# Kernel optimization log

Measured on AMD Instinct MI355X. Metric: run time of the kernel, lower is better.

## Reference

```python
import jax, jax.numpy as jnp
import numpy as np

N = 4096      # n_patches / nodes
IN_FEAT = 512
EMBED = 512
HEADS = 8
HEAD_DIM = EMBED // HEADS
SCALING = HEAD_DIM ** -0.5


def setup_inputs() -> dict:
    key = jax.random.key(0)
    ks = jax.random.split(key, 7)
    x = jax.random.normal(ks[0], (N, IN_FEAT), dtype=jnp.float32)
    adj = jax.random.randint(ks[1], (N, N), 0, 2, dtype=jnp.int32)
    s = 0.04  # ~xavier scale for 512x512
    WQ = jax.random.normal(ks[2], (EMBED, IN_FEAT), dtype=jnp.float32) * s
    WK = jax.random.normal(ks[3], (EMBED, IN_FEAT), dtype=jnp.float32) * s
    WV = jax.random.normal(ks[4], (EMBED, IN_FEAT), dtype=jnp.float32) * s
    we = jax.random.normal(ks[5], (1, HEAD_DIM), dtype=jnp.float32) * 0.1
    be = jnp.zeros((1,), dtype=jnp.float32)
    return {"x": x, "adj": adj, "WQ": WQ, "WK": WK, "WV": WV, "we": we, "be": be}


def reference(x, adj, WQ, WK, WV, we, be):
    n = x.shape[0]
    # projections: [N, E] -> [H, N, head_dim]
    Q = (x @ WQ.T).reshape(n, HEADS, HEAD_DIM).transpose(1, 0, 2)
    K = (x @ WK.T).reshape(n, HEADS, HEAD_DIM).transpose(1, 0, 2)
    V = (x @ WV.T).reshape(n, HEADS, HEAD_DIM).transpose(1, 0, 2)
    # scores + per-query energy term: [H, N, N]
    energy = Q @ we.T + be                      # [H, N, 1]
    attn = jnp.einsum('hqd,hkd->hqk', Q, K) * SCALING + energy
    # adjacency mask (broadcast over heads)
    attn = attn + jnp.where(adj > 0, 0.0, -jnp.inf)
    attn = jax.nn.softmax(attn, axis=-1)
    # winner-take-all: one-hot at row max, divided by num_heads
    hard = (attn == jnp.max(attn, axis=-1, keepdims=True)).astype(jnp.float32) / HEADS
    out = jnp.einsum('hqk,hkd->hqd', hard, V)   # [H, N, head_dim]
    return out.transpose(1, 0, 2).reshape(n, EMBED)
```

## Files before the change

### kernel.cpp

```cpp
#include <hip/hip_runtime.h>
#include <hip/hip_bf16.h>
#include <float.h>
#include <stdint.h>

#define NPT    4096
#define EMB    512
#define NH     8
#define HD     64
#define KSPLIT 32

typedef __attribute__((ext_vector_type(8))) short bf16x8;
typedef __attribute__((ext_vector_type(4))) float f32x4;
typedef uint32_t u32;

__device__ __forceinline__ void async_ld16(const void* gsrc, void* ldst) {
    __builtin_amdgcn_global_load_lds(
        (const __attribute__((address_space(1))) u32*)gsrc,
        (__attribute__((address_space(3))) u32*)ldst, 16, 0, 0);
}

__device__ __forceinline__ void split3(float a, unsigned short& h,
                                       unsigned short& m, unsigned short& l) {
    __hip_bfloat16 bh = __float2bfloat16(a);
    float fh = __bfloat162float(bh);
    float r1 = a - fh;
    __hip_bfloat16 bm = __float2bfloat16(r1);
    float fm = __bfloat162float(bm);
    float r2 = r1 - fm;
    __hip_bfloat16 bl = __float2bfloat16(r2);
    h = *reinterpret_cast<unsigned short*>(&bh);
    m = *reinterpret_cast<unsigned short*>(&bm);
    l = *reinterpret_cast<unsigned short*>(&bl);
}

__global__ __launch_bounds__(256) void prep_kernel(const float* __restrict__ x,
                                                   const float* __restrict__ wq,
                                                   const float* __restrict__ wk,
                                                   const float* __restrict__ wv,
                                                   const int* __restrict__ adj,
                                                   unsigned short* __restrict__ xs,
                                                   unsigned short* __restrict__ wqs,
                                                   unsigned short* __restrict__ wks,
                                                   unsigned short* __restrict__ wvs,
                                                   unsigned* __restrict__ bits_t) {
    int y = blockIdx.y;
    size_t i = (size_t)blockIdx.x * 256 + threadIdx.x;
    if (y == 4) {
        int q = (int)(i >> 7), w = (int)i & 127;
        const int4* p = (const int4*)(adj + (size_t)q * NPT + w * 32);
        unsigned m = 0;
#pragma unroll
        for (int j = 0; j < 8; ++j) {
            int4 v = p[j];
            m |= (v.x != 0 ? 1u : 0u) << (j * 4 + 0);
            m |= (v.y != 0 ? 1u : 0u) << (j * 4 + 1);
            m |= (v.z != 0 ? 1u : 0u) << (j * 4 + 2);
            m |= (v.w != 0 ? 1u : 0u) << (j * 4 + 3);
        }
        bits_t[(size_t)w * NPT + q] = m;
    } else if (y == 0) {
        const size_t PL = (size_t)NPT * EMB;
        float4 v = ((const float4*)x)[i];
        int n  = (int)(i >> 7);
        int k0 = ((int)i & 127) * 4;
        int kc = k0 >> 5, kg = (k0 >> 3) & 3, dd = k0 & 7;
        size_t off = ((((size_t)(n >> 4) * 16 + kc) * 4 + kg) * 16 + (n & 15)) * 8 + dd;
        ushort4 h, m, l;
        split3(v.x, h.x, m.x, l.x);
        split3(v.y, h.y, m.y, l.y);
        split3(v.z, h.z, m.z, l.z);
        split3(v.w, h.w, m.w, l.w);
        *(ushort4*)(xs + off)          = h;
        *(ushort4*)(xs + PL + off)     = m;
        *(ushort4*)(xs + 2 * PL + off) = l;
    } else {
        const size_t WPL = 262144;
        if (i >= WPL / 4) return;
        const float* src = (y == 1) ? wq : (y == 2) ? wk : wv;
        unsigned short* dst = (y == 1) ? wqs : (y == 2) ? wks : wvs;
        float4 v = ((const float4*)src)[i];
        int e  = (int)(i >> 7);
        int k0 = ((int)i & 127) * 4;
        int ebk = e >> 6, el = e & 63;
        int kc = k0 >> 5, g = (k0 >> 3) & 3, dd = k0 & 7;
        size_t off = ((((size_t)ebk * 16 + kc) * 4 + g) * 64 + el) * 8 + dd;
        ushort4 h, m, l;
        split3(v.x, h.x, m.x, l.x);
        split3(v.y, h.y, m.y, l.y);
        split3(v.z, h.z, m.z, l.z);
        split3(v.w, h.w, m.w, l.w);
        *(ushort4*)(dst + off)           = h;
        *(ushort4*)(dst + WPL + off)     = m;
        *(ushort4*)(dst + 2 * WPL + off) = l;
    }
}

__global__ __launch_bounds__(256) void gemm_mfma(const unsigned short* __restrict__ xs,
                                                 const unsigned short* __restrict__ wqs,
                                                 const unsigned short* __restrict__ wks,
                                                 const unsigned short* __restrict__ wvs,
                                                 unsigned short* __restrict__ Q3,
                                                 unsigned short* __restrict__ K3,
                                                 float* __restrict__ V) {
    const size_t XPL = (size_t)NPT * EMB;
    const size_t WPL = 262144;
    const size_t OPL = (size_t)NH * NPT * HD;

    const int tn  = blockIdx.x;
    const int ebk = blockIdx.y;
    const int tid = threadIdx.x;
    const int wv = tid >> 6, lane = tid & 63;
    const int wn = wv & 1, we = wv >> 1;
    const int m = lane & 15, quad = lane >> 4;
    const int n0 = tn * 128 + wn * 64;
    const int e0 = we * 32;

    __shared__ __align__(16) unsigned short Ws[3 * 3 * 4 * 64 * 8];

    const unsigned short* Wz[3] = {wqs, wks, wvs};

    f32x4 acc[3][2][4];
#pragma unroll
    for (int z = 0; z < 3; ++z)
#pragma unroll
        for (int mt = 0; mt < 2; ++mt)
#pragma unroll
            for (int nt = 0; nt < 4; ++nt) acc[z][mt][nt] = (f32x4){0.f, 0.f, 0.f, 0.f};

#pragma unroll 1
    for (int kc = 0; kc < 16; ++kc) {
        __syncthreads();
#pragma unroll
        for (int i2 = 0; i2 < 9; ++i2) {
            int c = wv + 4 * i2;
            int z = c / 12, p = (c / 4) % 3, kg = c & 3;
            const unsigned short* src = Wz[z] + (size_t)p * WPL
                + (((size_t)ebk * 16 + kc) * 4 + kg) * 512 + lane * 8;
            async_ld16(src, &Ws[((z * 3 + p) * 4 + kg) * 512]);
        }
        bf16x8 xf[4][3];
#pragma unroll
        for (int nt = 0; nt < 4; ++nt) {
            int tni = tn * 8 + wn * 4 + nt;
#pragma unroll
            for (int p = 0; p < 3; ++p)
                xf[nt][p] = *(const bf16x8*)(xs + (size_t)p * XPL
                    + ((((size_t)tni * 16 + kc) * 4 + quad) * 16 + m) * 8);
        }
        __syncthreads();

#pragma unroll
        for (int ga = 0; ga < 3; ++ga) {
#pragma unroll
            for (int z = 0; z < 3; ++z) {
                bf16x8 af[2];
#pragma unroll
                for (int mt = 0; mt < 2; ++mt)
                    af[mt] = *(const bf16x8*)
                        &Ws[(((z * 3 + ga) * 4 + quad) * 64 + e0 + mt * 16 + m) * 8];
#pragma unroll
                for (int pb = 0; pb < 3 - ga; ++pb)
#pragma unroll
                    for (int mt = 0; mt < 2; ++mt)
#pragma unroll
                        for (int nt = 0; nt < 4; ++nt)
                            acc[z][mt][nt] = __builtin_amdgcn_mfma_f32_16x16x32_bf16(
                                af[mt], xf[nt][pb], acc[z][mt][nt], 0, 0, 0);
            }
        }
    }

    const int h = ebk;
#pragma unroll
    for (int z = 0; z < 3; ++z)
#pragma unroll
        for (int mt = 0; mt < 2; ++mt)
#pragma unroll
            for (int nt = 0; nt < 4; ++nt) {
                const int n = n0 + nt * 16 + m;
                const int dL = e0 + mt * 16 + quad * 4;
                f32x4 a = acc[z][mt][nt];
                if (z == 2) {
                    *(f32x4*)(V + (size_t)n * EMB + ebk * 64 + dL) = a;
                } else {
                    ushort4 ph, pm, pl;
                    split3(a[0], ph.x, pm.x, pl.x);
                    split3(a[1], ph.y, pm.y, pl.y);
                    split3(a[2], ph.z, pm.z, pl.z);
                    split3(a[3], ph.w, pm.w, pl.w);
                    unsigned short* O3 = (z == 0) ? Q3 : K3;
                    size_t off = ((size_t)h * 128 + (n >> 5)) * 2048
                               + (dL >> 3) * 256 + (n & 31) * 8 + (dL & 7);
                    *(ushort4*)(O3 + off)           = ph;
                    *(ushort4*)(O3 + OPL + off)     = pm;
                    *(ushort4*)(O3 + 2 * OPL + off) = pl;
                }
            }
}

__global__ __launch_bounds__(256) void score_mfma(const unsigned short* __restrict__ Q3,
                                                  const unsigned short* __restrict__ K3,
                                                  const unsigned* __restrict__ bits_t,
                                                  float* __restrict__ pval,
                                                  int* __restrict__ pidx) {
    const int qb = blockIdx.x * 128;
    const int ks = blockIdx.y;
    const int tid = threadIdx.x;
    const int wv = tid >> 6, lane = tid & 63;
    const int m = lane & 15, quad = lane >> 4;
    const size_t PL = (size_t)NH * NPT * HD;
    const int kq = qb + wv * 32;

    __shared__ __align__(16) unsigned short Ks[3][3 * 2048];

    auto prefetchK = [&](int t) {
        int h = t >> 2, kt = ks * 4 + (t & 3), buf = t % 3;
#pragma unroll
        for (int i2 = 0; i2 < 3; ++i2) {
            int c = wv + 4 * i2;
            int p = c >> 2, sub = c & 3;
            const unsigned short* src = K3 + (size_t)p * PL
                + ((size_t)h * 128 + kt) * 2048 + (sub * 64 + lane) * 8;
            async_ld16(src, &Ks[buf][p * 2048 + sub * 512]);
        }
    };

    prefetchK(0);
    prefetchK(1);

    bf16x8 qf[2][2][3];
    float bestv[2]; int besti[2];

#pragma unroll 1
    for (int t = 0; t < NH * 4; ++t) {
        const int h = t >> 2, kst = t & 3, buf = t % 3;
        const int kbase = ks * 128 + kst * 32;

        asm volatile("s_waitcnt vmcnt(3)\n\ts_barrier" ::: "memory");

        if (kst == 0) {
#pragma unroll
            for (int nt = 0; nt < 2; ++nt)
#pragma unroll
                for (int dc = 0; dc < 2; ++dc)
#pragma unroll
                    for (int p = 0; p < 3; ++p)
                        qf[nt][dc][p] = *(const bf16x8*)(Q3 + (size_t)p * PL
                            + ((size_t)h * 128 + (kq >> 5)) * 2048
                            + (dc * 4 + quad) * 256 + (nt * 16 + m) * 8);
            bestv[0] = bestv[1] = -FLT_MAX;
            besti[0] = besti[1] = 0;
        }

        unsigned bw[2];
#pragma unroll
        for (int nt = 0; nt < 2; ++nt)
            bw[nt] = bits_t[(size_t)(ks * 4 + kst) * NPT + kq + nt * 16 + m];

        if (t + 2 < NH * 4) prefetchK(t + 2);

        f32x4 acc[2][2];
#pragma unroll
        for (int mt = 0; mt < 2; ++mt)
#pragma unroll
            for (int nt = 0; nt < 2; ++nt) acc[mt][nt] = (f32x4){0.f, 0.f, 0.f, 0.f};

#pragma unroll
        for (int ga = 0; ga < 3; ++ga) {
            bf16x8 kf[2][2];
#pragma unroll
            for (int mt = 0; mt < 2; ++mt)
#pragma unroll
                for (int dc = 0; dc < 2; ++dc)
                    kf[mt][dc] = *(const bf16x8*)
                        &Ks[buf][ga * 2048 + ((dc * 4 + quad) * 32 + mt * 16 + m) * 8];
#pragma unroll
            for (int pb = 0; pb < 3 - ga; ++pb)
#pragma unroll
                for (int dc = 0; dc < 2; ++dc)
#pragma unroll
                    for (int mt = 0; mt < 2; ++mt)
#pragma unroll
                        for (int nt = 0; nt < 2; ++nt)
                            acc[mt][nt] = __builtin_amdgcn_mfma_f32_16x16x32_bf16(
                                kf[mt][dc], qf[nt][dc][pb], acc[mt][nt], 0, 0, 0);
        }

#pragma unroll
        for (int nt = 0; nt < 2; ++nt) {
            unsigned w = bw[nt];
#pragma unroll
            for (int mt = 0; mt < 2; ++mt) {
                int k0 = mt * 16 + quad * 4;
                f32x4 a = acc[mt][nt];
#pragma unroll
                for (int r = 0; r < 4; ++r) {
                    if ((w >> (k0 + r)) & 1u) {
                        float s = a[r];
                        if (s > bestv[nt]) { bestv[nt] = s; besti[nt] = kbase + k0 + r; }
                    }
                }
            }
        }

        if (kst == 3) {
#pragma unroll
            for (int nt = 0; nt < 2; ++nt) {
                float v = bestv[nt]; int bi = besti[nt];
#pragma unroll
                for (int off = 16; off < 64; off <<= 1) {
                    float ov = __shfl_xor(v, off);
                    int   oi = __shfl_xor(bi, off);
                    if (ov > v || (ov == v && oi < bi)) { v = ov; bi = oi; }
                }
                if (quad == 0) {
                    size_t o = ((size_t)h * KSPLIT + ks) * NPT + kq + nt * 16 + m;
                    pval[o] = v; pidx[o] = bi;
                }
            }
        }
    }
}

__global__ __launch_bounds__(128) void gather_out(const float* __restrict__ V,
                                                  const float* __restrict__ pval,
                                                  const int* __restrict__ pidx,
                                                  float* __restrict__ out) {
    const int q = blockIdx.x;
    const int tid = threadIdx.x;
    __shared__ int widx[NH];
    if (tid < NH) {
        float bv = -FLT_MAX; int bi = 0;
        for (int ks = 0; ks < KSPLIT; ++ks) {
            size_t off = ((size_t)tid * KSPLIT + ks) * NPT + q;
            float v = pval[off];
            if (v > bv) { bv = v; bi = pidx[off]; }
        }
        widx[tid] = bi;
    }
    __syncthreads();
    const int h = tid >> 4;
    const int d4 = (tid & 15) * 4;
    const int k = widx[h];
    float4 v = *(const float4*)(V + (size_t)k * EMB + h * HD + d4);
    v.x *= 0.125f; v.y *= 0.125f; v.z *= 0.125f; v.w *= 0.125f;
    *(float4*)(out + (size_t)q * EMB + h * HD + d4) = v;
}

extern "C" void kernel_launch(void* const* d_in, const int* in_sizes, int n_in,
                              void* d_out, int out_size, void* d_ws, size_t ws_size,
                              hipStream_t stream) {
    const float* x   = (const float*)d_in[0];
    const int*   adj = (const int*)d_in[1];
    const float* WQ  = (const float*)d_in[2];
    const float* WK  = (const float*)d_in[3];
    const float* WV  = (const float*)d_in[4];
    float* out = (float*)d_out;

    char* ws = (char*)d_ws;
    const size_t HMB = 512u * 1024;
    unsigned short* xs   = (unsigned short*)(ws);
    unsigned short* wqs  = (unsigned short*)(ws + 24 * HMB);
    unsigned short* wks  = (unsigned short*)(ws + 27 * HMB);
    unsigned short* wvs  = (unsigned short*)(ws + 30 * HMB);
    unsigned short* Q3   = (unsigned short*)(ws + 33 * HMB);
    unsigned short* K3   = (unsigned short*)(ws + 57 * HMB);
    float*          V    = (float*)(ws + 81 * HMB);
    unsigned*       bits = (unsigned*)(ws + 97 * HMB);
    float*          pval = (float*)(ws);
    int*            pidx = (int*)(ws + 8 * HMB);

    prep_kernel<<<dim3(2048, 5), dim3(256), 0, stream>>>(x, WQ, WK, WV, adj,
                                                         xs, wqs, wks, wvs, bits);
    gemm_mfma<<<dim3(32, NH), dim3(256), 0, stream>>>(xs, wqs, wks, wvs, Q3, K3, V);
    score_mfma<<<dim3(NPT / 128, KSPLIT), dim3(256), 0, stream>>>(Q3, K3, bits, pval, pidx);
    gather_out<<<dim3(NPT), dim3(128), 0, stream>>>(V, pval, pidx, out);
}
```

Baseline: 278.8 us.

## Pipeline projection GEMM weight loads and split k-split reduction into coalesced kernel

The projection GEMM now streams weights through a triple-buffered LDS ring, one stage per (k-chunk, projection), prefetched two stages ahead with vmcnt-based waits. This replaces the two full barriers per iteration and overlaps global-to-LDS loads with MFMA work. The per-query argmax reduction over k-splits moves out of gather_out, where only 8 threads per block did serial strided loads, into a separate kernel where each thread handles one (head, query) with coalesced reads. This adds a kernel launch and a workspace buffer for the winner indices.

```diff
diff --git a/kernel.cpp b/kernel.cpp
--- a/kernel.cpp
+++ b/kernel.cpp
@@ -115,58 +115,69 @@
     const int n0 = tn * 128 + wn * 64;
     const int e0 = we * 32;
 
-    __shared__ __align__(16) unsigned short Ws[3 * 3 * 4 * 64 * 8];
+    __shared__ __align__(16) unsigned short Ws[3][6144];
 
     const unsigned short* Wz[3] = {wqs, wks, wvs};
 
-    f32x4 acc[3][2][4];
-#pragma unroll
-    for (int z = 0; z < 3; ++z)
-#pragma unroll
-        for (int mt = 0; mt < 2; ++mt)
-#pragma unroll
-            for (int nt = 0; nt < 4; ++nt) acc[z][mt][nt] = (f32x4){0.f, 0.f, 0.f, 0.f};
-
-#pragma unroll 1
-    for (int kc = 0; kc < 16; ++kc) {
-        __syncthreads();
-#pragma unroll
-        for (int i2 = 0; i2 < 9; ++i2) {
+    auto prefetchS = [&](int s) {
+        int kc = s / 3, z = s % 3, buf = s % 3 == s % 3 ? (s % 3) : 0;
+        buf = s % 3;
+#pragma unroll
+        for (int i2 = 0; i2 < 3; ++i2) {
             int c = wv + 4 * i2;
-            int z = c / 12, p = (c / 4) % 3, kg = c & 3;
+            int p = c >> 2, kg = c & 3;
             const unsigned short* src = Wz[z] + (size_t)p * WPL
                 + (((size_t)ebk * 16 + kc) * 4 + kg) * 512 + lane * 8;
-            async_ld16(src, &Ws[((z * 3 + p) * 4 + kg) * 512]);
-        }
-        bf16x8 xf[4][3];
-#pragma unroll
-        for (int nt = 0; nt < 4; ++nt) {
-            int tni = tn * 8 + wn * 4 + nt;
-#pragma unroll
-            for (int p = 0; p < 3; ++p)
-                xf[nt][p] = *(const bf16x8*)(xs + (size_t)p * XPL
-                    + ((((size_t)tni * 16 + kc) * 4 + quad) * 16 + m) * 8);
-        }
-        __syncthreads();
+            async_ld16(src, &Ws[buf][(p * 4 + kg) * 512]);
+        }
+    };
+
+    f32x4 acc[3][2][4];
+#pragma unroll
+    for (int z = 0; z < 3; ++z)
+#pragma unroll
+        for (int mt = 0; mt < 2; ++mt)
+#pragma unroll
+            for (int nt = 0; nt < 4; ++nt) acc[z][mt][nt] = (f32x4){0.f, 0.f, 0.f, 0.f};
+
+    prefetchS(0);
+    prefetchS(1);
+
+    bf16x8 xf[4][3];
+#pragma unroll 1
+    for (int s = 0; s < 48; ++s) {
+        const int kc = s / 3, z = s % 3, buf = s % 3;
+
+        if (s < 47) asm volatile("s_waitcnt vmcnt(3)\n\ts_barrier" ::: "memory");
+        else        asm volatile("s_waitcnt vmcnt(0)\n\ts_barrier" ::: "memory");
+
+        if (z == 0) {
+#pragma unroll
+            for (int nt = 0; nt < 4; ++nt) {
+                int tni = tn * 8 + wn * 4 + nt;
+#pragma unroll
+                for (int p = 0; p < 3; ++p)
+                    xf[nt][p] = *(const bf16x8*)(xs + (size_t)p * XPL
+                        + ((((size_t)tni * 16 + kc) * 4 + quad) * 16 + m) * 8);
+            }
+        }
+        if (s + 2 < 48) prefetchS(s + 2);
 
 #pragma unroll
         for (int ga = 0; ga < 3; ++ga) {
-#pragma unroll
-            for (int z = 0; z < 3; ++z) {
-                bf16x8 af[2];
+            bf16x8 af[2];
+#pragma unroll
+            for (int mt = 0; mt < 2; ++mt)
+                af[mt] = *(const bf16x8*)
+                    &Ws[buf][((ga * 4 + quad) * 64 + e0 + mt * 16 + m) * 8];
+#pragma unroll
+            for (int pb = 0; pb < 3 - ga; ++pb)
 #pragma unroll
                 for (int mt = 0; mt < 2; ++mt)
-                    af[mt] = *(const bf16x8*)
-                        &Ws[(((z * 3 + ga) * 4 + quad) * 64 + e0 + mt * 16 + m) * 8];
-#pragma unroll
-                for (int pb = 0; pb < 3 - ga; ++pb)
-#pragma unroll
-                    for (int mt = 0; mt < 2; ++mt)
-#pragma unroll
-                        for (int nt = 0; nt < 4; ++nt)
-                            acc[z][mt][nt] = __builtin_amdgcn_mfma_f32_16x16x32_bf16(
-                                af[mt], xf[nt][pb], acc[z][mt][nt], 0, 0, 0);
-            }
+#pragma unroll
+                    for (int nt = 0; nt < 4; ++nt)
+                        acc[z][mt][nt] = __builtin_amdgcn_mfma_f32_16x16x32_bf16(
+                            af[mt], xf[nt][pb], acc[z][mt][nt], 0, 0, 0);
         }
     }
 
@@ -322,26 +333,30 @@
     }
 }
 
+__global__ __launch_bounds__(256) void reduce_ksplit(const float* __restrict__ pval,
+                                                     const int* __restrict__ pidx,
+                                                     int* __restrict__ widx) {
+    const int q = blockIdx.x * 256 + threadIdx.x;
+    const int h = blockIdx.y;
+    float bv = -FLT_MAX; int bi = 0;
+#pragma unroll 4
+    for (int ks = 0; ks < KSPLIT; ++ks) {
+        size_t off = ((size_t)h * KSPLIT + ks) * NPT + q;
+        float v = pval[off];
+        int   d = pidx[off];
+        if (v > bv) { bv = v; bi = d; }
+    }
+    widx[(size_t)h * NPT + q] = bi;
+}
+
 __global__ __launch_bounds__(128) void gather_out(const float* __restrict__ V,
-                                                  const float* __restrict__ pval,
-                                                  const int* __restrict__ pidx,
+                                                  const int* __restrict__ widx,
                                                   float* __restrict__ out) {
     const int q = blockIdx.x;
     const int tid = threadIdx.x;
-    __shared__ int widx[NH];
-    if (tid < NH) {
-        float bv = -FLT_MAX; int bi = 0;
-        for (int ks = 0; ks < KSPLIT; ++ks) {
-            size_t off = ((size_t)tid * KSPLIT + ks) * NPT + q;
-            float v = pval[off];
-            if (v > bv) { bv = v; bi = pidx[off]; }
-        }
-        widx[tid] = bi;
-    }
-    __syncthreads();
     const int h = tid >> 4;
     const int d4 = (tid & 15) * 4;
-    const int k = widx[h];
+    const int k = widx[(size_t)h * NPT + q];
     float4 v = *(const float4*)(V + (size_t)k * EMB + h * HD + d4);
     v.x *= 0.125f; v.y *= 0.125f; v.z *= 0.125f; v.w *= 0.125f;
     *(float4*)(out + (size_t)q * EMB + h * HD + d4) = v;
@@ -367,6 +382,7 @@
     unsigned short* K3   = (unsigned short*)(ws + 57 * HMB);
     float*          V    = (float*)(ws + 81 * HMB);
     unsigned*       bits = (unsigned*)(ws + 97 * HMB);
+    int*            widx = (int*)(ws + 101 * HMB);
     float*          pval = (float*)(ws);
     int*            pidx = (int*)(ws + 8 * HMB);
 
@@ -374,5 +390,6 @@
                                                          xs, wqs, wks, wvs, bits);
     gemm_mfma<<<dim3(32, NH), dim3(256), 0, stream>>>(xs, wqs, wks, wvs, Q3, K3, V);
     score_mfma<<<dim3(NPT / 128, KSPLIT), dim3(256), 0, stream>>>(Q3, K3, bits, pval, pidx);
-    gather_out<<<dim3(NPT), dim3(128), 0, stream>>>(V, pval, pidx, out);
-}
+    reduce_ksplit<<<dim3(NPT / 256, NH), dim3(256), 0, stream>>>(pval, pidx, widx);
+    gather_out<<<dim3(NPT), dim3(128), 0, stream>>>(V, widx, out);
+}
```

Result: slower. 425.5 us (+52.6%).
